# Optimization experiments

Hardware: AMD Instinct MI355X
Metric: run time of the kernel (lower is better)

## Reference

```python
import jax, jax.numpy as jnp
import numpy as np

B, T, D = 2, 2048, 4096
H, HKV, HD = 32, 8, 128
N_REP = H // HKV
THETA = 500000.0


def _rope(x, cos, sin):
    # x: [B, T, h, HD]; cos/sin: [T, HD//2]
    xr = x.reshape(*x.shape[:-1], HD // 2, 2)
    x0, x1 = xr[..., 0], xr[..., 1]
    c = cos[None, :, None, :]
    s = sin[None, :, None, :]
    o0 = x0 * c - x1 * s
    o1 = x0 * s + x1 * c
    return jnp.stack([o0, o1], axis=-1).reshape(x.shape)


def setup_inputs() -> dict:
    key = jax.random.key(0)
    ks = jax.random.split(key, 8)
    x = jax.random.normal(ks[0], (B, T, D), dtype=jnp.float32)
    # true Llama RoPE angles
    inv_freq = 1.0 / (THETA ** (np.arange(0, HD, 2, dtype=np.float32) / HD))
    ang = np.outer(np.arange(T, dtype=np.float32), inv_freq)  # [T, HD//2]
    freqs_cos = jnp.asarray(np.cos(ang), dtype=jnp.float32)
    freqs_sin = jnp.asarray(np.sin(ang), dtype=jnp.float32)
    mask = jnp.zeros((T, T), dtype=jnp.float32)  # accepted but unused (as in source)
    cache_k = jnp.zeros((B, T, HKV, HD), dtype=jnp.float32)
    cache_v = jnp.zeros((B, T, HKV, HD), dtype=jnp.float32)
    sc = 0.02
    wq = jax.random.normal(ks[1], (D, H * HD), dtype=jnp.float32) * sc
    wk = jax.random.normal(ks[2], (D, HKV * HD), dtype=jnp.float32) * sc
    wv = jax.random.normal(ks[3], (D, HKV * HD), dtype=jnp.float32) * sc
    wo = jax.random.normal(ks[4], (H * HD, D), dtype=jnp.float32) * sc
    return {"x": x, "freqs_cos": freqs_cos, "freqs_sin": freqs_sin, "mask": mask,
            "cache_k": cache_k, "cache_v": cache_v,
            "wq": wq, "wk": wk, "wv": wv, "wo": wo, "start_pos": 0}


def reference(x, freqs_cos, freqs_sin, mask, cache_k, cache_v, wq, wk, wv, wo, start_pos):
    b, t, _ = x.shape
    q = (x @ wq).reshape(b, t, H, HD)
    k = (x @ wk).reshape(b, t, HKV, HD)
    v = (x @ wv).reshape(b, t, HKV, HD)
    q = _rope(q, freqs_cos, freqs_sin)
    k = _rope(k, freqs_cos, freqs_sin)
    # KV-cache write
    cache_k = jax.lax.dynamic_update_slice(cache_k, k, (0, start_pos, 0, 0))
    cache_v = jax.lax.dynamic_update_slice(cache_v, v, (0, start_pos, 0, 0))
    s_len = start_pos + t
    keys = jnp.repeat(cache_k[:, :s_len], N_REP, axis=2)    # [B, S, H, HD]
    values = jnp.repeat(cache_v[:, :s_len], N_REP, axis=2)  # [B, S, H, HD]
    # per-head scaled dot-product attention (vectorized over heads)
    scores = jnp.einsum('bthd,bshd->bhts', q, keys) / jnp.sqrt(jnp.float32(HD))
    probs = jax.nn.softmax(scores, axis=-1)  # mask is NOT applied in the source forward
    out = jnp.einsum('bhts,bshd->bthd', probs, values).reshape(b, t, H * HD)
    return out @ wo
```

## Files before the change

kernel.cpp:

```cpp
#include <hip/hip_runtime.h>

typedef unsigned short u16;
typedef unsigned int   u32;
typedef __attribute__((ext_vector_type(2))) unsigned int u32x2;
typedef __attribute__((ext_vector_type(4))) float f32x4;
typedef __attribute__((ext_vector_type(8))) short s16x8;
typedef __attribute__((ext_vector_type(4))) _Float16 f16x4;
typedef __attribute__((ext_vector_type(8))) _Float16 f16x8;

#define B_   2
#define T_   2048
#define D_   4096
#define H_   32
#define HKV_ 8
#define HD_  128
#define NQKV 6144
#define M_   (B_*T_)

__device__ __forceinline__ u16 f2bf(float f){
  u32 u = __float_as_uint(f);
  u += 0x7fffu + ((u >> 16) & 1u);
  return (u16)(u >> 16);
}
__device__ __forceinline__ float bf2f(u16 h){
  return __uint_as_float(((u32)h) << 16);
}
__device__ __forceinline__ void gload16(const void* g, void* l){
  __builtin_amdgcn_global_load_lds(
      (const __attribute__((address_space(1))) u32*)g,
      (__attribute__((address_space(3))) u32*)l, 16, 0, 0);
}

__global__ void k_convert_x(const float* __restrict__ in, u16* __restrict__ out){
  int i = blockIdx.x * 256 + threadIdx.x;
  float4 v = reinterpret_cast<const float4*>(in)[i];
  u32 lo = (u32)f2bf(v.x) | ((u32)f2bf(v.y) << 16);
  u32 hi = (u32)f2bf(v.z) | ((u32)f2bf(v.w) << 16);
  u32x2 p; p.x = lo; p.y = hi;
  reinterpret_cast<u32x2*>(out)[i] = p;
}

__global__ void k_transpose_w(const float* __restrict__ in, u16* __restrict__ out,
                              int K, int N){
  __shared__ float tile[64][65];
  int n0 = blockIdx.x * 64, k0 = blockIdx.y * 64;
  int tid = threadIdx.x;
  int tx = tid & 15, ty = tid >> 4;
  #pragma unroll
  for (int rr = 0; rr < 4; rr++) {
    int r = ty + 16 * rr;
    float4 v = *reinterpret_cast<const float4*>(in + (size_t)(k0 + r) * N + n0 + 4 * tx);
    tile[r][4 * tx + 0] = v.x; tile[r][4 * tx + 1] = v.y;
    tile[r][4 * tx + 2] = v.z; tile[r][4 * tx + 3] = v.w;
  }
  __syncthreads();
  #pragma unroll
  for (int ni = 0; ni < 4; ni++) {
    int nn = ty + 16 * ni;
    ushort4 o;
    o.x = f2bf(tile[4 * tx + 0][nn]);
    o.y = f2bf(tile[4 * tx + 1][nn]);
    o.z = f2bf(tile[4 * tx + 2][nn]);
    o.w = f2bf(tile[4 * tx + 3][nn]);
    *reinterpret_cast<ushort4*>(out + (size_t)(n0 + nn) * K + k0 + 4 * tx) = o;
  }
}

#define AS_(b) (smem + (b) * 65536)
#define BS_(b) (smem + (b) * 65536 + 32768)
#define BARX  asm volatile("s_barrier" ::: "memory")
#define PRIO1 __builtin_amdgcn_s_setprio(1)
#define PRIO0 __builtin_amdgcn_s_setprio(0)
#define VM4   asm volatile("s_waitcnt vmcnt(4)" ::: "memory")
#define VM0   asm volatile("s_waitcnt vmcnt(0)" ::: "memory")
#define LGKM0 do { asm volatile("s_waitcnt lgkmcnt(0)" ::: "memory"); \
                   __builtin_amdgcn_sched_barrier(0); } while (0)

#define STAGE_HA(buf, half, kt) { \
  _Pragma("unroll") for (int r2 = 0; r2 < 2; r2++) { \
    int rw = (half) * 128 + r2 * 64 + w * 8; \
    gload16(A + (size_t)(m0 + rw + subrow) * K + (kt) * 64 + srcoff, \
            AS_(buf) + rw * 128); } }
#define STAGE_HB(buf, half, kt) { \
  _Pragma("unroll") for (int r2 = 0; r2 < 2; r2++) { \
    int rw = (half) * 128 + r2 * 64 + w * 8; \
    gload16(Bt + (size_t)(n0 + rw + subrow) * K + (kt) * 64 + srcoff, \
            BS_(buf) + rw * 128); } }
#define RD_A2(buf, p) { \
  _Pragma("unroll") for (int rt = 0; rt < 2; rt++) { \
    int row = wr * 128 + (p) * 32 + rt * 16 + c; \
    const unsigned char* ptr = AS_(buf) + row * 128; \
    int sw = (row & 7) << 4; \
    af[rt][0] = *(const s16x8*)(ptr + ((16 * g) ^ sw)); \
    af[rt][1] = *(const s16x8*)(ptr + ((64 + 16 * g) ^ sw)); } }
#define RD_B8(buf) { \
  _Pragma("unroll") for (int ni = 0; ni < 4; ni++) { \
    int row = wc * 64 + ni * 16 + c; \
    const unsigned char* ptr = BS_(buf) + row * 128; \
    int sw = (row & 7) << 4; \
    bfr[ni][0] = *(const s16x8*)(ptr + ((16 * g) ^ sw)); \
    bfr[ni][1] = *(const s16x8*)(ptr + ((64 + 16 * g) ^ sw)); } }
#define MFP(p) { \
  _Pragma("unroll") for (int rt = 0; rt < 2; rt++) \
  _Pragma("unroll") for (int ni = 0; ni < 4; ni++) \
  _Pragma("unroll") for (int kk = 0; kk < 2; kk++) \
    acc[(p) * 2 + rt][ni] = __builtin_amdgcn_mfma_f32_16x16x32_bf16( \
        af[rt][kk], bfr[ni][kk], acc[(p) * 2 + rt][ni], 0, 0, 0); }

template<int OUT_F32>
__global__ __launch_bounds__(512, 1) void k_gemm8(
    const u16* __restrict__ A, const u16* __restrict__ Bt,
    void* __restrict__ Cv, int M, int N, int K)
{
  __shared__ __attribute__((aligned(16))) unsigned char smem[131072];
  const int tid = threadIdx.x;
  const int w = tid >> 6, l = tid & 63;
  const int c = l & 15, g = l >> 4;
  const int wr = w >> 2, wc = w & 3;

  const int nbx = N >> 8;
  const int nwg = nbx * (M >> 8);
  const int orig = blockIdx.x;
  const int id = (orig & 7) * (nwg >> 3) + (orig >> 3);
  const int m0 = (id / nbx) << 8;
  const int n0 = (id % nbx) << 8;

  const int srcoff = 8 * ((l & 7) ^ ((l >> 3) & 7));
  const int subrow = l >> 3;

  f32x4 acc[8][4];
  #pragma unroll
  for (int i = 0; i < 8; i++)
    #pragma unroll
    for (int j = 0; j < 4; j++)
      acc[i][j] = f32x4{0.f, 0.f, 0.f, 0.f};
  s16x8 af[2][2], bfr[4][2];

  STAGE_HB(0, 0, 0); STAGE_HB(0, 1, 0);
  STAGE_HA(0, 0, 0); STAGE_HA(0, 1, 0);
  STAGE_HB(1, 0, 1); STAGE_HB(1, 1, 1);
  VM4; BARX;

  const int NT2 = K >> 7;
  for (int it = 0; it < NT2; ++it) {
    const int tA = 2 * it, tB = 2 * it + 1;
    const bool st = (it < NT2 - 1);
    RD_A2(0, 0); RD_B8(0); STAGE_HA(1, 0, tB);
    BARX; LGKM0; PRIO1; MFP(0); PRIO0; BARX;
    RD_A2(0, 1); STAGE_HA(1, 1, tB);
    BARX; LGKM0; PRIO1; MFP(1); PRIO0; BARX;
    RD_A2(0, 2); if (st) STAGE_HB(0, 0, tA + 2);
    BARX; LGKM0; PRIO1; MFP(2); PRIO0; BARX;
    RD_A2(0, 3); if (st) STAGE_HB(0, 1, tA + 2);
    BARX; LGKM0; PRIO1; MFP(3); PRIO0;
    if (st) { VM4; } else { VM0; }
    BARX;
    RD_A2(1, 0); RD_B8(1); if (st) STAGE_HA(0, 0, tA + 2);
    BARX; LGKM0; PRIO1; MFP(0); PRIO0; BARX;
    RD_A2(1, 1); if (st) STAGE_HA(0, 1, tA + 2);
    BARX; LGKM0; PRIO1; MFP(1); PRIO0; BARX;
    RD_A2(1, 2); if (st) STAGE_HB(1, 0, tB + 2);
    BARX; LGKM0; PRIO1; MFP(2); PRIO0; BARX;
    RD_A2(1, 3); if (st) STAGE_HB(1, 1, tB + 2);
    BARX; LGKM0; PRIO1; MFP(3); PRIO0;
    if (st) { VM4; }
    BARX;
  }

  #pragma unroll
  for (int mi = 0; mi < 8; mi++)
    #pragma unroll
    for (int ni = 0; ni < 4; ni++)
      #pragma unroll
      for (int r = 0; r < 4; r++) {
        int m = m0 + wr * 128 + 16 * mi + 4 * g + r;
        int n = n0 + wc * 64 + 16 * ni + c;
        float v = acc[mi][ni][r];
        if (OUT_F32) reinterpret_cast<float*>(Cv)[(size_t)m * N + n] = v;
        else         reinterpret_cast<u16*>(Cv)[(size_t)m * N + n] = f2bf(v);
      }
}

__global__ void k_rope_q(u16* C1, const float* __restrict__ fc, const float* __restrict__ fs){
  int idx = blockIdx.x * 256 + threadIdx.x;
  int m = idx >> 11, p = idx & 2047;
  int h = p >> 6, i = p & 63;
  int t = m & (T_ - 1);
  u32* ptr = reinterpret_cast<u32*>(C1 + (size_t)m * NQKV + h * HD_ + 2 * i);
  u32 u = *ptr;
  float x0 = __uint_as_float(u << 16);
  float x1 = __uint_as_float(u & 0xffff0000u);
  float cc = fc[t * 64 + i], ss = fs[t * 64 + i];
  float o0 = x0 * cc - x1 * ss;
  float o1 = x0 * ss + x1 * cc;
  *ptr = (u32)f2bf(o0) | ((u32)f2bf(o1) << 16);
}

__global__ void k_rope_k(const u16* __restrict__ C1, const float* __restrict__ fc,
                         const float* __restrict__ fs, unsigned char* __restrict__ Kg){
  int idx = blockIdx.x * 256 + threadIdx.x;
  int m = idx >> 9, p = idx & 511;
  int kh = p >> 6, i = p & 63;
  int b = m >> 11, t = m & (T_ - 1);
  u32 u = *reinterpret_cast<const u32*>(C1 + (size_t)m * NQKV + D_ + kh * HD_ + 2 * i);
  float x0 = __uint_as_float(u << 16);
  float x1 = __uint_as_float(u & 0xffff0000u);
  float cc = fc[t * 64 + i], ss = fs[t * 64 + i];
  float o0 = x0 * cc - x1 * ss;
  float o1 = x0 * ss + x1 * cc;
  u32 packed = (u32)f2bf(o0) | ((u32)f2bf(o1) << 16);
  unsigned char* Kbb = Kg + (size_t)(b * HKV_ + kh) * 524288;
  int swb = (((i >> 2) ^ (t & 7)) << 4) | (4 * (i & 3));
  *reinterpret_cast<u32*>(Kbb + (size_t)t * 256 + swb) = packed;
}

__global__ void k_v_trans(const u16* __restrict__ C1, unsigned char* __restrict__ Vg){
  __shared__ float tile[32][33];
  int bz = blockIdx.z;
  int t0 = blockIdx.x * 32, d0 = blockIdx.y * 32;
  int tx = threadIdx.x, ty = threadIdx.y;
  int b = bz >> 3, kh = bz & 7;
  const u16* src = C1 + (size_t)(b * T_) * NQKV + D_ + HKV_ * HD_ + kh * HD_;
  #pragma unroll
  for (int i = ty; i < 32; i += 8)
    tile[i][tx] = bf2f(src[(size_t)(t0 + i) * NQKV + d0 + tx]);
  __syncthreads();
  unsigned char* Vbb = Vg + (size_t)bz * 524288;
  #pragma unroll
  for (int i = ty; i < 32; i += 8) {
    int d = d0 + i;
    int k = t0 + tx;
    int tt = k >> 6, kv = k & 63;
    int pp = (kv & 0x23) | ((kv & 0x10) >> 2) | ((kv & 0x0C) << 1);
    int swb = (((pp >> 3) ^ (d & 7)) << 4) | (2 * (pp & 7));
    *reinterpret_cast<_Float16*>(Vbb + (size_t)tt * 16384 + d * 128 + swb) =
        (_Float16)tile[tx][i];
  }
}

__global__ __launch_bounds__(256, 2) void k_attn(
    const u16* __restrict__ Q,
    const unsigned char* __restrict__ Kg,
    const unsigned char* __restrict__ Vg,
    u16* __restrict__ Ob)
{
  __shared__ __attribute__((aligned(16))) unsigned char smem[65536];
  const int tid = threadIdx.x;
  const int w = tid >> 6, l = tid & 63;
  const int c = l & 15, g = l >> 4;
  const int q0 = blockIdx.x * 128 + w * 32;
  const int h = blockIdx.y, b = blockIdx.z;
  const int kh = h >> 2;
  const unsigned char* Kb_ = Kg + (size_t)(b * HKV_ + kh) * 524288;
  const unsigned char* Vb_ = Vg + (size_t)(b * HKV_ + kh) * 524288;

  const float SCL2 = 0.08838834764831845f * 1.4426950408889634f;
  const float OFF2 = 14.4269504f;

  s16x8 qf[2][4];
  #pragma unroll
  for (int qt = 0; qt < 2; qt++)
    #pragma unroll
    for (int ci = 0; ci < 4; ci++)
      qf[qt][ci] = *reinterpret_cast<const s16x8*>(
          Q + (size_t)(b * T_ + q0 + 16 * qt + c) * NQKV + h * HD_ + 32 * ci + 8 * g);

  f32x4 o[2][8];
  #pragma unroll
  for (int qt = 0; qt < 2; qt++)
    #pragma unroll
    for (int i = 0; i < 8; i++) o[qt][i] = f32x4{0.f, 0.f, 0.f, 0.f};
  float lsum[2] = {0.f, 0.f};

  auto stage = [&](int bi, int tt) {
    const unsigned char* Ks = Kb_ + (size_t)tt * 16384;
    const unsigned char* Vs = Vb_ + (size_t)tt * 16384;
    unsigned char* Kl = smem + bi * 32768;
    unsigned char* Vl = Kl + 16384;
    #pragma unroll
    for (int i = 0; i < 4; i++) {
      int ch = i * 4 + w;
      gload16(Ks + ch * 1024 + l * 16, Kl + ch * 1024);
      gload16(Vs + ch * 1024 + l * 16, Vl + ch * 1024);
    }
  };

  stage(0, 0);
  asm volatile("s_waitcnt vmcnt(0)" ::: "memory");
  __syncthreads();

  for (int tt = 0; tt < T_ / 64; ++tt) {
    int cur = tt & 1;
    if (tt < T_ / 64 - 1) stage(cur ^ 1, tt + 1);
    const unsigned char* Kl = smem + cur * 32768;
    const unsigned char* Vl = Kl + 16384;

    f32x4 s[4][2];
    #pragma unroll
    for (int mi = 0; mi < 4; mi++)
      #pragma unroll
      for (int qt = 0; qt < 2; qt++) s[mi][qt] = f32x4{0.f, 0.f, 0.f, 0.f};

    #pragma unroll
    for (int mi = 0; mi < 4; mi++) {
      const int row = 16 * mi + c;
      const int sw = (row & 7) << 4;
      s16x8 kf[4];
      #pragma unroll
      for (int ci = 0; ci < 4; ci++)
        kf[ci] = *reinterpret_cast<const s16x8*>(Kl + row * 256 + ((64 * ci + 16 * g) ^ sw));
      #pragma unroll
      for (int qt = 0; qt < 2; qt++)
        #pragma unroll
        for (int ci = 0; ci < 4; ci++)
          s[mi][qt] = __builtin_amdgcn_mfma_f32_16x16x32_bf16(kf[ci], qf[qt][ci], s[mi][qt], 0, 0, 0);
    }

    f16x4 pa[2][4];
    #pragma unroll
    for (int qt = 0; qt < 2; qt++)
      #pragma unroll
      for (int mi = 0; mi < 4; mi++)
        #pragma unroll
        for (int r = 0; r < 4; r++) {
          float p = exp2f(s[mi][qt][r] * SCL2 - OFF2);
          lsum[qt] += p;
          pa[qt][mi][r] = (_Float16)p;
        }

    #pragma unroll
    for (int cp = 0; cp < 2; cp++)
      #pragma unroll
      for (int dc = 0; dc < 8; dc++) {
        const int d = 16 * dc + c;
        f16x8 v8 = *reinterpret_cast<const f16x8*>(
            Vl + d * 128 + ((64 * cp + 16 * g) ^ ((d & 7) << 4)));
        f16x4 lo = {v8[0], v8[1], v8[2], v8[3]};
        f16x4 hi = {v8[4], v8[5], v8[6], v8[7]};
        #pragma unroll
        for (int qt = 0; qt < 2; qt++) {
          o[qt][dc] = __builtin_amdgcn_mfma_f32_16x16x16f16(pa[qt][2 * cp], lo, o[qt][dc], 0, 0, 0);
          o[qt][dc] = __builtin_amdgcn_mfma_f32_16x16x16f16(pa[qt][2 * cp + 1], hi, o[qt][dc], 0, 0, 0);
        }
      }

    asm volatile("s_waitcnt vmcnt(0)" ::: "memory");
    __syncthreads();
  }

  #pragma unroll
  for (int qt = 0; qt < 2; qt++) {
    lsum[qt] += __shfl_xor(lsum[qt], 16);
    lsum[qt] += __shfl_xor(lsum[qt], 32);
  }
  float inv[2][4];
  #pragma unroll
  for (int qt = 0; qt < 2; qt++)
    #pragma unroll
    for (int r = 0; r < 4; r++)
      inv[qt][r] = 1.0f / __shfl(lsum[qt], 4 * g + r, 64);

  #pragma unroll
  for (int qt = 0; qt < 2; qt++) {
    u16* Orow = Ob + (size_t)(b * T_ + q0 + 16 * qt) * D_ + h * HD_;
    #pragma unroll
    for (int dc = 0; dc < 8; dc++)
      #pragma unroll
      for (int r = 0; r < 4; r++)
        Orow[(size_t)(4 * g + r) * D_ + 16 * dc + c] = f2bf(o[qt][dc][r] * inv[qt][r]);
  }
}

extern "C" void kernel_launch(void* const* d_in, const int* in_sizes, int n_in,
                              void* d_out, int out_size, void* d_ws, size_t ws_size,
                              hipStream_t stream)
{
  const float* x  = (const float*)d_in[0];
  const float* fc = (const float*)d_in[1];
  const float* fs = (const float*)d_in[2];
  const float* wq = (const float*)d_in[6];
  const float* wk = (const float*)d_in[7];
  const float* wv = (const float*)d_in[8];
  const float* wo = (const float*)d_in[9];

  unsigned char* w = (unsigned char*)d_ws;
  u16* Xb   = (u16*)(w);
  u16* Wt   = (u16*)(w + 33554432ull);
  u16* Wot  = (u16*)(w + 83886080ull);
  u16* C1   = (u16*)(w + 117440512ull);
  unsigned char* Kg = w + 167772160ull;
  unsigned char* Vg = w + 176160768ull;
  u16* Ob   = (u16*)(w + 184549376ull);

  k_convert_x<<<16384, 256, 0, stream>>>(x, Xb);
  k_transpose_w<<<dim3(64, 64), 256, 0, stream>>>(wq, Wt, D_, D_);
  k_transpose_w<<<dim3(16, 64), 256, 0, stream>>>(wk, Wt + (size_t)D_ * D_, D_, 1024);
  k_transpose_w<<<dim3(16, 64), 256, 0, stream>>>(wv, Wt + (size_t)5120 * D_, D_, 1024);
  k_transpose_w<<<dim3(64, 64), 256, 0, stream>>>(wo, Wot, D_, D_);

  k_gemm8<0><<<(NQKV / 256) * (M_ / 256), 512, 0, stream>>>(Xb, Wt, C1, M_, NQKV, D_);

  k_rope_q<<<32768, 256, 0, stream>>>(C1, fc, fs);
  k_rope_k<<<8192, 256, 0, stream>>>(C1, fc, fs, Kg);
  k_v_trans<<<dim3(64, 4, 16), dim3(32, 8), 0, stream>>>(C1, Vg);

  k_attn<<<dim3(T_ / 128, H_, B_), 256, 0, stream>>>(C1, Kg, Vg, Ob);

  k_gemm8<1><<<(D_ / 256) * (M_ / 256), 512, 0, stream>>>(Ob, Wot, d_out, M_, D_, D_);
}
```

Measured before the change: 579.1 us.

## Use simpler 128x128 single-buffered GEMM for QKV projection and raise MFMA priority in attention

Replaces the 256x256 double-buffered 8-wave GEMM used for the QKV projection with a new 128x128 tile, 4-wave, single-buffered kernel that has a two-blocks-per-CU launch bound. It also wraps the attention MFMA sequences with s_setprio(1)/s_setprio(0). The smaller tile raises block count and occupancy, but it drops the software pipelining and lowers data reuse per load, and it stores its output with scalar writes. The priority hints aim to give MFMA-issuing waves precedence while the CU is shared.

```diff
diff --git a/kernel.cpp b/kernel.cpp
--- a/kernel.cpp
+++ b/kernel.cpp
@@ -64,6 +64,75 @@
     o.w = f2bf(tile[4 * tx + 3][nn]);
     *reinterpret_cast<ushort4*>(out + (size_t)(n0 + nn) * K + k0 + 4 * tx) = o;
   }
+}
+
+template<int OUT_F32>
+__global__ __launch_bounds__(256, 2) void k_gemm(
+    const u16* __restrict__ A, const u16* __restrict__ Bt,
+    void* __restrict__ Cv, int M, int N, int K)
+{
+  __shared__ __attribute__((aligned(16))) unsigned char smem[32768];
+  unsigned char* As = smem;
+  unsigned char* Bs = smem + 16384;
+  const int tid = threadIdx.x;
+  const int w = tid >> 6, l = tid & 63;
+  const int m0 = blockIdx.y * 128, n0 = blockIdx.x * 128;
+  const int wm = (w >> 1) * 64, wn = (w & 1) * 64;
+  f32x4 acc[4][4];
+  #pragma unroll
+  for (int i = 0; i < 4; i++)
+    #pragma unroll
+    for (int j = 0; j < 4; j++)
+      acc[i][j] = f32x4{0.f, 0.f, 0.f, 0.f};
+
+  const int srcoff = 8 * ((l & 7) ^ ((l >> 3) & 7));
+  const int subrow = l >> 3;
+
+  for (int k0 = 0; k0 < K; k0 += 64) {
+    if (k0) __syncthreads();
+    #pragma unroll
+    for (int i = 0; i < 4; i++) {
+      int chunk = 4 * w + i;
+      int row = chunk * 8 + subrow;
+      gload16(A  + (size_t)(m0 + row) * K + k0 + srcoff, As + chunk * 1024);
+      gload16(Bt + (size_t)(n0 + row) * K + k0 + srcoff, Bs + chunk * 1024);
+    }
+    asm volatile("s_waitcnt vmcnt(0)" ::: "memory");
+    __syncthreads();
+    #pragma unroll
+    for (int kk = 0; kk < 2; kk++) {
+      s16x8 a[4], b[4];
+      const int co = kk * 64 + 16 * (l >> 4);
+      #pragma unroll
+      for (int mi = 0; mi < 4; mi++) {
+        int r = wm + 16 * mi + (l & 15);
+        a[mi] = *reinterpret_cast<const s16x8*>(As + r * 128 + (co ^ ((r & 7) << 4)));
+      }
+      #pragma unroll
+      for (int ni = 0; ni < 4; ni++) {
+        int r = wn + 16 * ni + (l & 15);
+        b[ni] = *reinterpret_cast<const s16x8*>(Bs + r * 128 + (co ^ ((r & 7) << 4)));
+      }
+      #pragma unroll
+      for (int mi = 0; mi < 4; mi++)
+        #pragma unroll
+        for (int ni = 0; ni < 4; ni++)
+          acc[mi][ni] = __builtin_amdgcn_mfma_f32_16x16x32_bf16(a[mi], b[ni], acc[mi][ni], 0, 0, 0);
+    }
+  }
+  const int g = l >> 4, c = l & 15;
+  #pragma unroll
+  for (int mi = 0; mi < 4; mi++)
+    #pragma unroll
+    for (int ni = 0; ni < 4; ni++)
+      #pragma unroll
+      for (int r = 0; r < 4; r++) {
+        int m = m0 + wm + 16 * mi + 4 * g + r;
+        int n = n0 + wn + 16 * ni + c;
+        float v = acc[mi][ni][r];
+        if (OUT_F32) reinterpret_cast<float*>(Cv)[(size_t)m * N + n] = v;
+        else         reinterpret_cast<u16*>(Cv)[(size_t)m * N + n] = f2bf(v);
+      }
 }
 
 #define AS_(b) (smem + (b) * 65536)
@@ -309,11 +378,13 @@
       #pragma unroll
       for (int ci = 0; ci < 4; ci++)
         kf[ci] = *reinterpret_cast<const s16x8*>(Kl + row * 256 + ((64 * ci + 16 * g) ^ sw));
+      __builtin_amdgcn_s_setprio(1);
       #pragma unroll
       for (int qt = 0; qt < 2; qt++)
         #pragma unroll
         for (int ci = 0; ci < 4; ci++)
           s[mi][qt] = __builtin_amdgcn_mfma_f32_16x16x32_bf16(kf[ci], qf[qt][ci], s[mi][qt], 0, 0, 0);
+      __builtin_amdgcn_s_setprio(0);
     }
 
     f16x4 pa[2][4];
@@ -337,11 +408,13 @@
             Vl + d * 128 + ((64 * cp + 16 * g) ^ ((d & 7) << 4)));
         f16x4 lo = {v8[0], v8[1], v8[2], v8[3]};
         f16x4 hi = {v8[4], v8[5], v8[6], v8[7]};
+        __builtin_amdgcn_s_setprio(1);
         #pragma unroll
         for (int qt = 0; qt < 2; qt++) {
           o[qt][dc] = __builtin_amdgcn_mfma_f32_16x16x16f16(pa[qt][2 * cp], lo, o[qt][dc], 0, 0, 0);
           o[qt][dc] = __builtin_amdgcn_mfma_f32_16x16x16f16(pa[qt][2 * cp + 1], hi, o[qt][dc], 0, 0, 0);
         }
+        __builtin_amdgcn_s_setprio(0);
       }
 
     asm volatile("s_waitcnt vmcnt(0)" ::: "memory");
@@ -398,7 +471,7 @@
   k_transpose_w<<<dim3(16, 64), 256, 0, stream>>>(wv, Wt + (size_t)5120 * D_, D_, 1024);
   k_transpose_w<<<dim3(64, 64), 256, 0, stream>>>(wo, Wot, D_, D_);
 
-  k_gemm8<0><<<(NQKV / 256) * (M_ / 256), 512, 0, stream>>>(Xb, Wt, C1, M_, NQKV, D_);
+  k_gemm<0><<<dim3(NQKV / 128, M_ / 128), 256, 0, stream>>>(Xb, Wt, C1, M_, NQKV, D_);
 
   k_rope_q<<<32768, 256, 0, stream>>>(C1, fc, fs);
   k_rope_k<<<8192, 256, 0, stream>>>(C1, fc, fs, Kg);
```

Measured after the change: 599.5 us. 3.5% more time.

## Use 128x256 tiles for QKV GEMM and 32-wide f16 MFMA in attention PV

Applied to the files above, without the earlier changes.

Adds a half-height GEMM kernel with 128x256 tiles and a smaller LDS footprint for the QKV projection, doubling the workgroup count to improve CU load balance and tail behavior. The attention PV product now uses the 16x16x32 f16 MFMA instead of two 16x16x16 instructions, removing vector shuffles and halving the instruction count. Smaller tiles reduce data reuse per block.

```diff
diff --git a/kernel.cpp b/kernel.cpp
--- a/kernel.cpp
+++ b/kernel.cpp
@@ -66,8 +66,6 @@
   }
 }
 
-#define AS_(b) (smem + (b) * 65536)
-#define BS_(b) (smem + (b) * 65536 + 32768)
 #define BARX  asm volatile("s_barrier" ::: "memory")
 #define PRIO1 __builtin_amdgcn_s_setprio(1)
 #define PRIO0 __builtin_amdgcn_s_setprio(0)
@@ -76,6 +74,106 @@
 #define LGKM0 do { asm volatile("s_waitcnt lgkmcnt(0)" ::: "memory"); \
                    __builtin_amdgcn_sched_barrier(0); } while (0)
 
+#define HAS_(b) (smem + (b) * 49152)
+#define HBS_(b) (smem + (b) * 49152 + 16384)
+#define H_STAGE_A(buf, half, kt) { \
+    int rw = (half) * 64 + w * 8; \
+    gload16(A + (size_t)(m0 + rw + subrow) * K + (kt) * 64 + srcoff, \
+            HAS_(buf) + rw * 128); }
+#define H_STAGE_B(buf, half, kt) { \
+  _Pragma("unroll") for (int r2 = 0; r2 < 2; r2++) { \
+    int rw = (half) * 128 + r2 * 64 + w * 8; \
+    gload16(Bt + (size_t)(n0 + rw + subrow) * K + (kt) * 64 + srcoff, \
+            HBS_(buf) + rw * 128); } }
+#define H_RD_A2(buf, p) { \
+  _Pragma("unroll") for (int rt = 0; rt < 2; rt++) { \
+    int row = wr * 64 + (p) * 32 + rt * 16 + c; \
+    const unsigned char* ptr = HAS_(buf) + row * 128; \
+    int sw = (row & 7) << 4; \
+    af[rt][0] = *(const s16x8*)(ptr + ((16 * g) ^ sw)); \
+    af[rt][1] = *(const s16x8*)(ptr + ((64 + 16 * g) ^ sw)); } }
+#define H_RD_B8(buf) { \
+  _Pragma("unroll") for (int ni = 0; ni < 4; ni++) { \
+    int row = wc * 64 + ni * 16 + c; \
+    const unsigned char* ptr = HBS_(buf) + row * 128; \
+    int sw = (row & 7) << 4; \
+    bfr[ni][0] = *(const s16x8*)(ptr + ((16 * g) ^ sw)); \
+    bfr[ni][1] = *(const s16x8*)(ptr + ((64 + 16 * g) ^ sw)); } }
+#define H_MFP(p) { \
+  _Pragma("unroll") for (int rt = 0; rt < 2; rt++) \
+  _Pragma("unroll") for (int ni = 0; ni < 4; ni++) \
+  _Pragma("unroll") for (int kk = 0; kk < 2; kk++) \
+    acc[(p) * 2 + rt][ni] = __builtin_amdgcn_mfma_f32_16x16x32_bf16( \
+        af[rt][kk], bfr[ni][kk], acc[(p) * 2 + rt][ni], 0, 0, 0); }
+
+__global__ __launch_bounds__(512, 1) void k_gemm8h(
+    const u16* __restrict__ A, const u16* __restrict__ Bt,
+    u16* __restrict__ Cv, int M, int N, int K)
+{
+  __shared__ __attribute__((aligned(16))) unsigned char smem[98304];
+  const int tid = threadIdx.x;
+  const int w = tid >> 6, l = tid & 63;
+  const int c = l & 15, g = l >> 4;
+  const int wr = w >> 2, wc = w & 3;
+
+  const int nbx = N >> 8;
+  const int nwg = nbx * (M >> 7);
+  const int orig = blockIdx.x;
+  const int id = (orig & 7) * (nwg >> 3) + (orig >> 3);
+  const int m0 = (id / nbx) << 7;
+  const int n0 = (id % nbx) << 8;
+
+  const int srcoff = 8 * ((l & 7) ^ ((l >> 3) & 7));
+  const int subrow = l >> 3;
+
+  f32x4 acc[4][4];
+  #pragma unroll
+  for (int i = 0; i < 4; i++)
+    #pragma unroll
+    for (int j = 0; j < 4; j++)
+      acc[i][j] = f32x4{0.f, 0.f, 0.f, 0.f};
+  s16x8 af[2][2], bfr[4][2];
+
+  H_STAGE_B(0, 0, 0); H_STAGE_B(0, 1, 0);
+  H_STAGE_A(0, 0, 0); H_STAGE_A(0, 1, 0);
+  H_STAGE_B(1, 0, 1); H_STAGE_B(1, 1, 1);
+  VM4; BARX;
+
+  const int NT2 = K >> 7;
+  for (int it = 0; it < NT2; ++it) {
+    const int tA = 2 * it, tB = 2 * it + 1;
+    const bool st = (it < NT2 - 1);
+    H_RD_A2(0, 0); H_RD_B8(0); H_STAGE_A(1, 0, tB); H_STAGE_A(1, 1, tB);
+    BARX; LGKM0; PRIO1; H_MFP(0); PRIO0; BARX;
+    H_RD_A2(0, 1);
+    if (st) { H_STAGE_B(0, 0, tA + 2); H_STAGE_B(0, 1, tA + 2); }
+    BARX; LGKM0; PRIO1; H_MFP(1); PRIO0;
+    if (st) { VM4; } else { VM0; }
+    BARX;
+    H_RD_A2(1, 0); H_RD_B8(1);
+    if (st) { H_STAGE_A(0, 0, tA + 2); H_STAGE_A(0, 1, tA + 2); }
+    BARX; LGKM0; PRIO1; H_MFP(0); PRIO0; BARX;
+    H_RD_A2(1, 1);
+    if (st) { H_STAGE_B(1, 0, tB + 2); H_STAGE_B(1, 1, tB + 2); }
+    BARX; LGKM0; PRIO1; H_MFP(1); PRIO0;
+    if (st) { VM4; }
+    BARX;
+  }
+
+  #pragma unroll
+  for (int mi = 0; mi < 4; mi++)
+    #pragma unroll
+    for (int ni = 0; ni < 4; ni++)
+      #pragma unroll
+      for (int r = 0; r < 4; r++) {
+        int m = m0 + wr * 64 + 16 * mi + 4 * g + r;
+        int n = n0 + wc * 64 + 16 * ni + c;
+        Cv[(size_t)m * N + n] = f2bf(acc[mi][ni][r]);
+      }
+}
+
+#define AS_(b) (smem + (b) * 65536)
+#define BS_(b) (smem + (b) * 65536 + 32768)
 #define STAGE_HA(buf, half, kt) { \
   _Pragma("unroll") for (int r2 = 0; r2 < 2; r2++) { \
     int rw = (half) * 128 + r2 * 64 + w * 8; \
@@ -107,10 +205,9 @@
     acc[(p) * 2 + rt][ni] = __builtin_amdgcn_mfma_f32_16x16x32_bf16( \
         af[rt][kk], bfr[ni][kk], acc[(p) * 2 + rt][ni], 0, 0, 0); }
 
-template<int OUT_F32>
 __global__ __launch_bounds__(512, 1) void k_gemm8(
     const u16* __restrict__ A, const u16* __restrict__ Bt,
-    void* __restrict__ Cv, int M, int N, int K)
+    float* __restrict__ Cv, int M, int N, int K)
 {
   __shared__ __attribute__((aligned(16))) unsigned char smem[131072];
   const int tid = threadIdx.x;
@@ -175,9 +272,7 @@
       for (int r = 0; r < 4; r++) {
         int m = m0 + wr * 128 + 16 * mi + 4 * g + r;
         int n = n0 + wc * 64 + 16 * ni + c;
-        float v = acc[mi][ni][r];
-        if (OUT_F32) reinterpret_cast<float*>(Cv)[(size_t)m * N + n] = v;
-        else         reinterpret_cast<u16*>(Cv)[(size_t)m * N + n] = f2bf(v);
+        Cv[(size_t)m * N + n] = acc[mi][ni][r];
       }
 }
 
@@ -316,7 +411,7 @@
           s[mi][qt] = __builtin_amdgcn_mfma_f32_16x16x32_bf16(kf[ci], qf[qt][ci], s[mi][qt], 0, 0, 0);
     }
 
-    f16x4 pa[2][4];
+    f16x8 pa8[2][2];
     #pragma unroll
     for (int qt = 0; qt < 2; qt++)
       #pragma unroll
@@ -325,7 +420,7 @@
         for (int r = 0; r < 4; r++) {
           float p = exp2f(s[mi][qt][r] * SCL2 - OFF2);
           lsum[qt] += p;
-          pa[qt][mi][r] = (_Float16)p;
+          pa8[qt][mi >> 1][(mi & 1) * 4 + r] = (_Float16)p;
         }
 
     #pragma unroll
@@ -335,13 +430,9 @@
         const int d = 16 * dc + c;
         f16x8 v8 = *reinterpret_cast<const f16x8*>(
             Vl + d * 128 + ((64 * cp + 16 * g) ^ ((d & 7) << 4)));
-        f16x4 lo = {v8[0], v8[1], v8[2], v8[3]};
-        f16x4 hi = {v8[4], v8[5], v8[6], v8[7]};
         #pragma unroll
-        for (int qt = 0; qt < 2; qt++) {
-          o[qt][dc] = __builtin_amdgcn_mfma_f32_16x16x16f16(pa[qt][2 * cp], lo, o[qt][dc], 0, 0, 0);
-          o[qt][dc] = __builtin_amdgcn_mfma_f32_16x16x16f16(pa[qt][2 * cp + 1], hi, o[qt][dc], 0, 0, 0);
-        }
+        for (int qt = 0; qt < 2; qt++)
+          o[qt][dc] = __builtin_amdgcn_mfma_f32_16x16x32_f16(pa8[qt][cp], v8, o[qt][dc], 0, 0, 0);
       }
 
     asm volatile("s_waitcnt vmcnt(0)" ::: "memory");
@@ -398,7 +489,7 @@
   k_transpose_w<<<dim3(16, 64), 256, 0, stream>>>(wv, Wt + (size_t)5120 * D_, D_, 1024);
   k_transpose_w<<<dim3(64, 64), 256, 0, stream>>>(wo, Wot, D_, D_);
 
-  k_gemm8<0><<<(NQKV / 256) * (M_ / 256), 512, 0, stream>>>(Xb, Wt, C1, M_, NQKV, D_);
+  k_gemm8h<<<(NQKV / 256) * (M_ / 128), 512, 0, stream>>>(Xb, Wt, C1, M_, NQKV, D_);
 
   k_rope_q<<<32768, 256, 0, stream>>>(C1, fc, fs);
   k_rope_k<<<8192, 256, 0, stream>>>(C1, fc, fs, Kg);
@@ -406,5 +497,5 @@
 
   k_attn<<<dim3(T_ / 128, H_, B_), 256, 0, stream>>>(C1, Kg, Vg, Ob);
 
-  k_gemm8<1><<<(D_ / 256) * (M_ / 256), 512, 0, stream>>>(Ob, Wot, d_out, M_, D_, D_);
-}
+  k_gemm8<<<(D_ / 256) * (M_ / 256), 512, 0, stream>>>(Ob, Wot, (float*)d_out, M_, D_, D_);
+}
```

Measured after the change: 580.1 us. About the same (+0.2%).
